# Kernel tuning notes

Hardware: AMD Instinct MI355X
Metric: run time of the kernel (lower is better)

Reference implementation:

```python
import jax, jax.numpy as jnp
import numpy as np

L, K, D, V, S, B = 2, 4, 1024, 32000, 1024, 2

# Constant neighbor influence from the 2x2 grid (success_rate==0.5 for fresh blocks)
_pos = np.array([[0, 0], [0, 1], [1, 0], [1, 1]], dtype=np.float64)
_dist = np.sqrt(((_pos[:, None, :] - _pos[None, :, :]) ** 2).sum(-1))
_infl = np.where(np.eye(K, dtype=bool), 0.0, 0.5 / (1.0 + _dist)).sum(-1)
NEIGHBOR_SIG = jnp.asarray(1.0 / (1.0 + np.exp(-_infl)), dtype=jnp.float32)  # [K]


def _ln(x, g, b, eps=1e-5):
    mu = x.mean(-1, keepdims=True)
    var = ((x - mu) ** 2).mean(-1, keepdims=True)
    return (x - mu) / jnp.sqrt(var + eps) * g + b


def setup_inputs() -> dict:
    key = jax.random.key(0)
    ks = jax.random.split(key, 10)
    def n(k, shape, s):
        return jax.random.normal(k, shape, jnp.float32) * s
    return {
        "input_ids": jax.random.randint(ks[0], (B, S), 0, V),
        "embedding": n(ks[1], (V, D), 0.02),
        "pos_enc": n(ks[2], (S, D), 0.02),
        "torsion_field": jnp.zeros((D,), jnp.float32),
        "ln1_g": jnp.ones((L, D), jnp.float32),
        "ln1_b": jnp.zeros((L, D), jnp.float32),
        "base_W": n(ks[3], (L, D, D), 0.02),
        "blk_W1": n(ks[4], (L, K, D // 2, D), 0.02),
        "blk_W2": n(ks[5], (L, K, D, D // 2), 0.02),
        "blk_gate": n(ks[6], (L, K, D), 0.01),
        "prop_W": n(ks[7], (L, K, K), 0.5),
        "prop_b": jnp.zeros((L, K), jnp.float32),
        "ln2_g": jnp.ones((L, D), jnp.float32),
        "ln2_b": jnp.zeros((L, D), jnp.float32),
        "out_ln_g": jnp.ones((D,), jnp.float32),
        "out_ln_b": jnp.zeros((D,), jnp.float32),
        "lm_head_W": n(ks[8], (V, D), 0.02),
    }


def reference(input_ids, embedding, pos_enc, torsion_field, ln1_g, ln1_b,
              base_W, blk_W1, blk_W2, blk_gate, prop_W, prop_b,
              ln2_g, ln2_b, out_ln_g, out_ln_b, lm_head_W):
    h = embedding[input_ids] + pos_enc[None]  # [B,S,D]
    s = jnp.full((K,), 0.5, h.dtype)  # fresh blocks: success_rate = 0.5
    for l in range(L):
        # excitement (detached in torch via .item())
        exc0 = jax.nn.sigmoid(prop_W[l] @ s + prop_b[l])
        exc = jax.lax.stop_gradient(0.6 * exc0 + 0.4 * NEIGHBOR_SIG)  # [K]
        hn = _ln(h, ln1_g[l], ln1_b[l])
        base = hn @ base_W[l].T  # [B,S,D]
        # all K blocks are always loaded (min_blocks == max_blocks == 4)
        t = jnp.einsum('bsd,khd->bksh', hn, blk_W1[l])
        t = jax.nn.gelu(t, approximate=False)
        t = jnp.einsum('bksh,kdh->bksd', t, blk_W2[l])
        gate = jax.nn.sigmoid(blk_gate[l] + torsion_field)  # [K,D]
        t = t * gate[None, :, None, :]
        combined = jnp.einsum('bksd,k->bsd', t, exc) / exc.sum()
        h = h + (base + combined) * 0.3
        h = _ln(h, ln2_g[l], ln2_b[l])
    h = _ln(h, out_ln_g, out_ln_b)
    return h @ lm_head_W.T  # [B,S,V]
```

## Files before the change

### kernel.cpp

```cpp
#include <hip/hip_runtime.h>
#include <math.h>

typedef unsigned short u16;
typedef short s16x8 __attribute__((ext_vector_type(8)));
typedef float f32x4 __attribute__((ext_vector_type(4)));
typedef u16 u16x4 __attribute__((ext_vector_type(4)));
typedef int i32x4 __attribute__((ext_vector_type(4)));

#define D 1024
#define MM 2048
#define HH 512
#define VV 32000

static __device__ __forceinline__ u16 f2bf(float f) {
    union { float f; unsigned int i; } c; c.f = f;
    unsigned int x = c.i;
    return (u16)((x + 0x7fffu + ((x >> 16) & 1u)) >> 16);
}
static __device__ __forceinline__ float sigm(float x) { return 1.0f / (1.0f + expf(-x)); }

static __device__ __forceinline__ void load_lds16(const u16* g, u16* l) {
    __builtin_amdgcn_global_load_lds(
        (const __attribute__((address_space(1))) unsigned int*)g,
        (__attribute__((address_space(3))) unsigned int*)l, 16, 0, 0);
}

__global__ __launch_bounds__(256) void cvt_kernel(const float* __restrict__ in,
                                                  u16* __restrict__ out, const int n4)
{
    for (int i = blockIdx.x * 256 + threadIdx.x; i < n4; i += gridDim.x * 256) {
        f32x4 v = ((const f32x4*)in)[i];
        u16x4 o;
#pragma unroll
        for (int j = 0; j < 4; j++) o[j] = f2bf(v[j]);
        ((u16x4*)out)[i] = o;
    }
}

__global__ __launch_bounds__(256) void embed_kernel(const int* __restrict__ ids,
    const float* __restrict__ emb, const float* __restrict__ pos, float* __restrict__ h)
{
    const int m = blockIdx.x;
    const int s = m & 1023;
    const long id = ids[m];
    const int d = threadIdx.x * 4;
    f32x4 ev = *(const f32x4*)&emb[id * D + d];
    f32x4 pv = *(const f32x4*)&pos[(long)s * D + d];
    f32x4 o;
#pragma unroll
    for (int i = 0; i < 4; i++) o[i] = ev[i] + pv[i];
    *(f32x4*)&h[(long)m * D + d] = o;
}

__global__ __launch_bounds__(256) void ln_bf16_kernel(const float* __restrict__ h,
    u16* __restrict__ out, const float* __restrict__ g, const float* __restrict__ b)
{
    const int row = blockIdx.x;
    const int d = threadIdx.x * 4;
    f32x4 x = *(const f32x4*)&h[(long)row * D + d];
    float s = x[0] + x[1] + x[2] + x[3];
    float ss = x[0]*x[0] + x[1]*x[1] + x[2]*x[2] + x[3]*x[3];
#pragma unroll
    for (int off = 32; off; off >>= 1) { s += __shfl_xor(s, off); ss += __shfl_xor(ss, off); }
    __shared__ float red[8];
    const int wid = threadIdx.x >> 6;
    if ((threadIdx.x & 63) == 0) { red[wid] = s; red[4 + wid] = ss; }
    __syncthreads();
    s = red[0] + red[1] + red[2] + red[3];
    ss = red[4] + red[5] + red[6] + red[7];
    const float mu = s * (1.0f / D);
    const float rstd = rsqrtf(ss * (1.0f / D) - mu * mu + 1e-5f);
    f32x4 gv = *(const f32x4*)&g[d];
    f32x4 bv = *(const f32x4*)&b[d];
    u16x4 o;
#pragma unroll
    for (int i = 0; i < 4; i++) o[i] = f2bf((x[i] - mu) * rstd * gv[i] + bv[i]);
    *(u16x4*)&out[(long)row * D + d] = o;
}

__global__ __launch_bounds__(256) void resln_kernel(float* __restrict__ h,
    const float* __restrict__ c, const float* __restrict__ g, const float* __restrict__ b)
{
    const int row = blockIdx.x;
    const int d = threadIdx.x * 4;
    f32x4 x = *(const f32x4*)&h[(long)row * D + d];
    f32x4 cv = *(const f32x4*)&c[(long)row * D + d];
#pragma unroll
    for (int i = 0; i < 4; i++) x[i] += 0.3f * cv[i];
    float s = x[0] + x[1] + x[2] + x[3];
    float ss = x[0]*x[0] + x[1]*x[1] + x[2]*x[2] + x[3]*x[3];
#pragma unroll
    for (int off = 32; off; off >>= 1) { s += __shfl_xor(s, off); ss += __shfl_xor(ss, off); }
    __shared__ float red[8];
    const int wid = threadIdx.x >> 6;
    if ((threadIdx.x & 63) == 0) { red[wid] = s; red[4 + wid] = ss; }
    __syncthreads();
    s = red[0] + red[1] + red[2] + red[3];
    ss = red[4] + red[5] + red[6] + red[7];
    const float mu = s * (1.0f / D);
    const float rstd = rsqrtf(ss * (1.0f / D) - mu * mu + 1e-5f);
    f32x4 gv = *(const f32x4*)&g[d];
    f32x4 bv = *(const f32x4*)&b[d];
    f32x4 o;
#pragma unroll
    for (int i = 0; i < 4; i++) o[i] = (x[i] - mu) * rstd * gv[i] + bv[i];
    *(f32x4*)&h[(long)row * D + d] = o;
}

__global__ void exc_kernel(const float* __restrict__ pW, const float* __restrict__ pb,
                           float* __restrict__ sc)
{
    if (threadIdx.x == 0 && blockIdx.x == 0) {
        const float NS = 1.0f / (1.0f + expf(-0.70710678118654752f));
        float e[4], sum = 0.0f;
        for (int k = 0; k < 4; k++) {
            float a = pb[k];
            for (int j = 0; j < 4; j++) a += 0.5f * pW[k * 4 + j];
            e[k] = 0.6f * sigm(a) + 0.4f * NS;
            sum += e[k];
        }
        for (int k = 0; k < 4; k++) sc[k] = e[k] / sum;
    }
}

__global__ __launch_bounds__(256) void scale_w2_kernel(
    const float* __restrict__ W2l,
    const float* __restrict__ gatel,
    const float* __restrict__ tors,
    const float* __restrict__ sc,
    u16* __restrict__ W2eff)
{
    const int n = blockIdx.x >> 1;
    const int half = blockIdx.x & 1;
    const int kh = half * 1024 + threadIdx.x * 4;
    const int k = kh >> 9;
    const int hh = kh & 511;
    const float f = sigm(gatel[k * D + n] + tors[n]) * sc[k];
    f32x4 w = *(const f32x4*)&W2l[((long)k * D + n) * HH + hh];
    u16x4 o;
#pragma unroll
    for (int i = 0; i < 4; i++) o[i] = f2bf(w[i] * f);
    *(u16x4*)&W2eff[(long)n * 2048 + kh] = o;
}

template<int EPI, int BN>
__global__ __launch_bounds__(256) void gemm_lds_kernel(
    const u16* __restrict__ A, const u16* __restrict__ W,
    float* __restrict__ Cf, u16* __restrict__ Cb,
    const int K, const long ldc, const long strideWz, const long strideCz)
{
    W += (long)blockIdx.z * strideWz;
    if (EPI == 1) Cb += (long)blockIdx.z * strideCz;
    else          Cf += (long)blockIdx.z * strideCz;

    const int gx = gridDim.x;
    const int nwg = gx * gridDim.y;
    int lin = blockIdx.y * gx + blockIdx.x;
    lin = (lin & 7) * (nwg >> 3) + (lin >> 3);
    const int bm = (lin % gx) * 128;
    const int bn = (lin / gx) * BN;

    __shared__ __align__(16) u16 As[128 * 32];
    __shared__ __align__(16) u16 Bs[BN * 32];

    const int tid = threadIdx.x;
    const int lane = tid & 63;
    const int w = tid >> 6;
    const int wm = (w >> 1) * 64;
    const int wn = (w & 1) * (BN / 2);
    const int lr = lane & 15;
    const int lkb = (lane >> 4) * 16;

    const int srow = lane >> 2;
    const int scol = (lane & 3) * 8;

    constexpr int NA = 8;
    constexpr int NB = BN / 16;
    constexpr int NIT = (NA + NB) / 4;

    f32x4 acc[4][BN / 32];
#pragma unroll
    for (int i = 0; i < 4; i++)
#pragma unroll
        for (int j = 0; j < BN / 32; j++) acc[i][j] = f32x4{0.f, 0.f, 0.f, 0.f};

    for (int k0 = 0; k0 < K; k0 += 32) {
        __syncthreads();
#pragma unroll
        for (int it = 0; it < NIT; ++it) {
            const int c = w + it * 4;
            if (c < NA) {
                load_lds16(&A[(long)(bm + c * 16 + srow) * K + k0 + scol], &As[c * 512]);
            } else {
                const int c2 = c - NA;
                load_lds16(&W[(long)(bn + c2 * 16 + srow) * K + k0 + scol], &Bs[c2 * 512]);
            }
        }
        __syncthreads();
        s16x8 a[4], b[BN / 32];
#pragma unroll
        for (int i = 0; i < 4; i++)
            a[i] = *(const s16x8*)((const char*)As + (wm + i * 16 + lr) * 64 + lkb);
#pragma unroll
        for (int j = 0; j < BN / 32; j++)
            b[j] = *(const s16x8*)((const char*)Bs + (wn + j * 16 + lr) * 64 + lkb);
#pragma unroll
        for (int i = 0; i < 4; i++)
#pragma unroll
            for (int j = 0; j < BN / 32; j++)
                acc[i][j] = __builtin_amdgcn_mfma_f32_16x16x32_bf16(a[i], b[j], acc[i][j], 0, 0, 0);
    }

    const int r0 = (lane >> 4) * 4;
#pragma unroll
    for (int i = 0; i < 4; i++) {
#pragma unroll
        for (int j = 0; j < BN / 32; j++) {
            const int n = bn + wn + j * 16 + lr;
#pragma unroll
            for (int r = 0; r < 4; r++) {
                const int m = bm + wm + i * 16 + r0 + r;
                const float v = acc[i][j][r];
                if (EPI == 0) {
                    Cf[(long)m * ldc + n] = v;
                } else if (EPI == 1) {
                    const float gel = 0.5f * v * (1.0f + erff(v * 0.70710678118654752f));
                    Cb[(long)m * ldc + n] = f2bf(gel);
                } else {
                    Cf[(long)m * ldc + n] += v;
                }
            }
        }
    }
}

extern "C" void kernel_launch(void* const* d_in, const int* in_sizes, int n_in,
                              void* d_out, int out_size, void* d_ws, size_t ws_size,
                              hipStream_t stream)
{
    (void)in_sizes; (void)n_in; (void)out_size; (void)ws_size;
    const int*   ids   = (const int*)d_in[0];
    const float* emb   = (const float*)d_in[1];
    const float* pos   = (const float*)d_in[2];
    const float* tors  = (const float*)d_in[3];
    const float* ln1g  = (const float*)d_in[4];
    const float* ln1b  = (const float*)d_in[5];
    const float* baseW = (const float*)d_in[6];
    const float* W1    = (const float*)d_in[7];
    const float* W2    = (const float*)d_in[8];
    const float* gate  = (const float*)d_in[9];
    const float* propW = (const float*)d_in[10];
    const float* propb = (const float*)d_in[11];
    const float* ln2g  = (const float*)d_in[12];
    const float* ln2b  = (const float*)d_in[13];
    const float* outg  = (const float*)d_in[14];
    const float* outb  = (const float*)d_in[15];
    const float* lmW   = (const float*)d_in[16];

    char* ws = (char*)d_ws;
    float* h     = (float*)(ws);
    u16*   hn    = (u16*)  (ws + (8l  << 20));
    u16*   bWbf  = (u16*)  (ws + (12l << 20));
    u16*   W1bf  = (u16*)  (ws + (14l << 20));
    float* C     = (float*)(ws + (18l << 20));
    u16*   t     = (u16*)  (ws + (26l << 20));
    u16*   W2eff = (u16*)  (ws + (34l << 20));
    float* sc    = (float*)(ws + (38l << 20));
    u16*   lmWbf = (u16*)  (ws + (12l << 20));

    embed_kernel<<<MM, 256, 0, stream>>>(ids, emb, pos, h);

    for (int l = 0; l < 2; l++) {
        exc_kernel<<<1, 64, 0, stream>>>(propW + l * 16, propb + l * 4, sc);
        ln_bf16_kernel<<<MM, 256, 0, stream>>>(h, hn, ln1g + (long)l * D, ln1b + (long)l * D);
        cvt_kernel<<<1024, 256, 0, stream>>>(baseW + (long)l * D * D, bWbf, D * D / 4);
        cvt_kernel<<<2048, 256, 0, stream>>>(W1 + (long)l * 4 * HH * D, W1bf, 4 * HH * D / 4);
        gemm_lds_kernel<0, 64><<<dim3(16, 16, 1), 256, 0, stream>>>(
            hn, bWbf, C, nullptr, D, D, 0, 0);
        gemm_lds_kernel<1, 64><<<dim3(16, 8, 4), 256, 0, stream>>>(
            hn, W1bf, nullptr, t, D, 2048, (long)HH * D, 512);
        scale_w2_kernel<<<2048, 256, 0, stream>>>(
            W2 + (long)l * 4 * D * HH, gate + (long)l * 4 * D, tors, sc, W2eff);
        gemm_lds_kernel<2, 64><<<dim3(16, 16, 1), 256, 0, stream>>>(
            t, W2eff, C, nullptr, 2048, D, 0, 0);
        resln_kernel<<<MM, 256, 0, stream>>>(h, C, ln2g + (long)l * D, ln2b + (long)l * D);
    }

    ln_bf16_kernel<<<MM, 256, 0, stream>>>(h, hn, outg, outb);
    cvt_kernel<<<2048, 256, 0, stream>>>(lmW, lmWbf, VV * D / 4);
    gemm_lds_kernel<0, 128><<<dim3(16, 250, 1), 256, 0, stream>>>(
        hn, lmWbf, (float*)d_out, nullptr, D, VV, 0, 0);
}
```

Before: 438.7 us.

## Add 256x256 pipelined LDS GEMM with XCD-aware tiling for LM head

Replaces the generic LM-head GEMM with a dedicated 512-thread kernel that computes 256x256 output tiles. It uses eight XOR-swizzled LDS slots with a ping-pong schedule that interleaves global-to-LDS loads with MFMA phases, plus s_setprio and explicit vmcnt waits. The block index is remapped so neighbouring tiles land on the same XCD, improving L2 reuse. The goal is higher MFMA utilisation and fewer stalls on the dominant 2048x32000x1024 GEMM, at the cost of hard-coded shapes and a large register footprint.

```diff
diff --git a/kernel.cpp b/kernel.cpp
--- a/kernel.cpp
+++ b/kernel.cpp
@@ -124,10 +124,8 @@
 }
 
 __global__ __launch_bounds__(256) void scale_w2_kernel(
-    const float* __restrict__ W2l,
-    const float* __restrict__ gatel,
-    const float* __restrict__ tors,
-    const float* __restrict__ sc,
+    const float* __restrict__ W2l, const float* __restrict__ gatel,
+    const float* __restrict__ tors, const float* __restrict__ sc,
     u16* __restrict__ W2eff)
 {
     const int n = blockIdx.x >> 1;
@@ -232,6 +230,111 @@
             }
         }
     }
+}
+
+
+static __device__ __forceinline__ void stageHalf(u16* slot, const u16* g, int wid, int lane) {
+    const int r = wid * 16 + (lane >> 2);
+    const int c16 = (lane & 3) ^ ((lane >> 2) & 3);
+    load_lds16(g + (long)r * 1024 + c16 * 8, slot + wid * 512);
+}
+static __device__ __forceinline__ s16x8 ldsFrag(const u16* slot, int fr, int lane) {
+    const int row = fr + (lane & 15);
+    const int c16 = (lane >> 4) ^ (row & 3);
+    return *(const s16x8*)(slot + row * 32 + c16 * 8);
+}
+
+#define SLOT(ab, buf, half) (lds[((ab) << 2) | ((buf) << 1) | (half)])
+#define VMCNT2() asm volatile("s_waitcnt vmcnt(2)" ::: "memory")
+#define SBAR()   do { __builtin_amdgcn_s_barrier(); __builtin_amdgcn_sched_barrier(0); } while (0)
+
+#define PHASE(qm, qn, rb, STAGE_STMT, DO_VM)                                        \
+    do {                                                                            \
+        s16x8 af[2], bf[4];                                                         \
+        _Pragma("unroll") for (int ii = 0; ii < 2; ++ii)                            \
+            af[ii] = ldsFrag(SLOT(0, rb, qm), fmBase + ii * 16, lane);              \
+        _Pragma("unroll") for (int jj = 0; jj < 4; ++jj)                            \
+            bf[jj] = ldsFrag(SLOT(1, rb, qn), fnBase + jj * 16, lane);              \
+        STAGE_STMT;                                                                 \
+        SBAR();                                                                     \
+        __builtin_amdgcn_s_setprio(1);                                              \
+        _Pragma("unroll") for (int ii = 0; ii < 2; ++ii)                            \
+            _Pragma("unroll") for (int jj = 0; jj < 4; ++jj)                        \
+                acc[qm][qn][ii][jj] = __builtin_amdgcn_mfma_f32_16x16x32_bf16(      \
+                    af[ii], bf[jj], acc[qm][qn][ii][jj], 0, 0, 0);                  \
+        __builtin_amdgcn_s_setprio(0);                                              \
+        if (DO_VM) VMCNT2();                                                        \
+        SBAR();                                                                     \
+    } while (0)
+
+__global__ __launch_bounds__(512, 2) void gemm256_kernel(
+    const u16* __restrict__ Ag, const u16* __restrict__ Wg, float* __restrict__ C)
+{
+    const int nwg = gridDim.x * gridDim.y;
+    int lin = blockIdx.y * gridDim.x + blockIdx.x;
+    lin = (lin & 7) * (nwg >> 3) + (lin >> 3);
+    const int bm = (lin & 7) * 256;
+    const int bn = (lin >> 3) * 256;
+
+    __shared__ __align__(16) u16 lds[8][128 * 32];
+
+    const int tid = threadIdx.x;
+    const int lane = tid & 63;
+    const int w = tid >> 6;
+    const int fmBase = (w & 3) * 32;
+    const int fnBase = (w >> 2) * 64;
+
+    f32x4 acc[2][2][2][4];
+#pragma unroll
+    for (int a0 = 0; a0 < 2; ++a0)
+#pragma unroll
+        for (int a1 = 0; a1 < 2; ++a1)
+#pragma unroll
+            for (int a2 = 0; a2 < 2; ++a2)
+#pragma unroll
+                for (int a3 = 0; a3 < 4; ++a3) acc[a0][a1][a2][a3] = f32x4{0.f, 0.f, 0.f, 0.f};
+
+    stageHalf(SLOT(0, 0, 0), Ag + (long)(bm      ) * 1024,      w, lane);
+    stageHalf(SLOT(1, 0, 0), Wg + (long)(bn      ) * 1024,      w, lane);
+    stageHalf(SLOT(0, 0, 1), Ag + (long)(bm + 128) * 1024,      w, lane);
+    stageHalf(SLOT(1, 0, 1), Wg + (long)(bn + 128) * 1024,      w, lane);
+    stageHalf(SLOT(1, 1, 0), Wg + (long)(bn      ) * 1024 + 32, w, lane);
+    stageHalf(SLOT(0, 1, 0), Ag + (long)(bm      ) * 1024 + 32, w, lane);
+    VMCNT2();
+    SBAR();
+
+    for (int i = 0; i < 16; ++i) {
+        const int t = 2 * i;
+        const long k1 = (long)(t + 1) * 32;
+        const long k2 = (long)((t + 2) & 31) * 32;
+        const long k3 = (long)((t + 3) & 31) * 32;
+
+        PHASE(0, 0, 0, stageHalf(SLOT(0, 1, 1), Ag + (long)(bm + 128) * 1024 + k1, w, lane), 0);
+        PHASE(1, 0, 0, stageHalf(SLOT(1, 1, 1), Wg + (long)(bn + 128) * 1024 + k1, w, lane), 0);
+        PHASE(0, 1, 0, stageHalf(SLOT(1, 0, 0), Wg + (long)(bn      ) * 1024 + k2, w, lane), 0);
+        PHASE(1, 1, 0, stageHalf(SLOT(0, 0, 0), Ag + (long)(bm      ) * 1024 + k2, w, lane), 1);
+        PHASE(0, 0, 1, stageHalf(SLOT(0, 0, 1), Ag + (long)(bm + 128) * 1024 + k2, w, lane), 0);
+        PHASE(1, 0, 1, stageHalf(SLOT(1, 0, 1), Wg + (long)(bn + 128) * 1024 + k2, w, lane), 0);
+        PHASE(0, 1, 1, stageHalf(SLOT(1, 1, 0), Wg + (long)(bn      ) * 1024 + k3, w, lane), 0);
+        PHASE(1, 1, 1, stageHalf(SLOT(0, 1, 0), Ag + (long)(bm      ) * 1024 + k3, w, lane), 1);
+    }
+
+    const int r0 = (lane >> 4) * 4;
+    const int cl = lane & 15;
+#pragma unroll
+    for (int qm = 0; qm < 2; ++qm)
+#pragma unroll
+        for (int qn = 0; qn < 2; ++qn)
+#pragma unroll
+            for (int ii = 0; ii < 2; ++ii)
+#pragma unroll
+                for (int jj = 0; jj < 4; ++jj) {
+                    const int m = bm + qm * 128 + fmBase + ii * 16 + r0;
+                    const int n = bn + qn * 128 + fnBase + jj * 16 + cl;
+#pragma unroll
+                    for (int rr = 0; rr < 4; ++rr)
+                        C[(long)(m + rr) * VV + n] = acc[qm][qn][ii][jj][rr];
+                }
 }
 
 extern "C" void kernel_launch(void* const* d_in, const int* in_sizes, int n_in,
@@ -288,6 +391,5 @@
 
     ln_bf16_kernel<<<MM, 256, 0, stream>>>(h, hn, outg, outb);
     cvt_kernel<<<2048, 256, 0, stream>>>(lmW, lmWbf, VV * D / 4);
-    gemm_lds_kernel<0, 128><<<dim3(16, 250, 1), 256, 0, stream>>>(
-        hn, lmWbf, (float*)d_out, nullptr, D, VV, 0, 0);
-}
+    gemm256_kernel<<<dim3(8, 125), 512, 0, stream>>>(hn, lmWbf, (float*)d_out);
+}
```

Result: slower. 451.7 us (+3.0%).

## Add 256x256-tile pipelined MFMA GEMM for the LM head projection

Applied to the files above, without the earlier changes.

Replaces the generic 128-wide LDS GEMM used for the final vocab projection with a dedicated 512-thread kernel. Each workgroup computes a 256x256 output tile using double-buffered global-to-LDS loads interleaved with MFMA phases. It also adds priority raising around the MFMA phases and a swizzled workgroup order for L2 reuse. The larger tiles cut global re-reads of the 2048x1024 activations and 32000x1024 weights, in exchange for a 128 KB LDS footprint, higher register pressure and many barriers per k-tile. The new kernel is hardcoded to M=2048, K=1024 and N=32000.

```diff
diff --git a/kernel.cpp b/kernel.cpp
--- a/kernel.cpp
+++ b/kernel.cpp
@@ -124,10 +124,8 @@
 }
 
 __global__ __launch_bounds__(256) void scale_w2_kernel(
-    const float* __restrict__ W2l,
-    const float* __restrict__ gatel,
-    const float* __restrict__ tors,
-    const float* __restrict__ sc,
+    const float* __restrict__ W2l, const float* __restrict__ gatel,
+    const float* __restrict__ tors, const float* __restrict__ sc,
     u16* __restrict__ W2eff)
 {
     const int n = blockIdx.x >> 1;
@@ -232,6 +230,139 @@
             }
         }
     }
+}
+
+
+#define AU16  16384
+#define HALFU 8192
+#define BB0   32768
+
+#define BAR() do { __builtin_amdgcn_s_barrier(); __builtin_amdgcn_sched_barrier(0); } while (0)
+
+__global__ __launch_bounds__(512, 2) void gemm256_kernel(
+    const u16* __restrict__ Ag, const u16* __restrict__ Wg, float* __restrict__ C)
+{
+    __shared__ __align__(16) u16 lds[65536];
+
+    const int nwg = gridDim.x * gridDim.y;
+    int lin = blockIdx.y * gridDim.x + blockIdx.x;
+    lin = (lin & 7) * (nwg >> 3) + (lin >> 3);
+    const int bm = (lin & 7) * 256;
+    const int bn = (lin >> 3) * 256;
+
+    const int tid = threadIdx.x;
+    const int lane = tid & 63;
+    const int w = tid >> 6;
+    const int wm = w >> 2;
+    const int wn = w & 3;
+
+    const u16* aSrc = Ag + (long)(bm + w * 16 + (lane & 15)) * 1024 + ((lane >> 4) * 8);
+    const u16* bSrc = Wg + (long)(bn + w * 16 + (lane & 15)) * 1024 + ((lane >> 4) * 8);
+    u16* aDst = lds + w * 1024;
+    u16* bDst = lds + BB0 + w * 1024;
+
+    auto stageA = [&](int kt, int b, int kk) {
+        const long co = (long)kt * 64 + kk * 32;
+        load_lds16(aSrc + co,               aDst + b * AU16 + kk * 512);
+        load_lds16(aSrc + co + 128 * 1024L, aDst + b * AU16 + HALFU + kk * 512);
+    };
+    auto stageB = [&](int kt, int b, int kk) {
+        const long co = (long)kt * 64 + kk * 32;
+        load_lds16(bSrc + co,               bDst + b * AU16 + kk * 512);
+        load_lds16(bSrc + co + 128 * 1024L, bDst + b * AU16 + HALFU + kk * 512);
+    };
+
+    const u16* aRd = lds + wm * HALFU + lane * 8;
+    const u16* bRd = lds + BB0 + (wn >> 1) * HALFU + (wn & 1) * 4096 + lane * 8;
+
+    f32x4 acc[8][4];
+#pragma unroll
+    for (int i = 0; i < 8; ++i)
+#pragma unroll
+        for (int j = 0; j < 4; ++j) acc[i][j] = f32x4{0.f, 0.f, 0.f, 0.f};
+
+    stageA(0, 0, 0); stageB(0, 0, 0); stageA(0, 0, 1); stageB(0, 0, 1);
+    stageA(1, 1, 0); stageB(1, 1, 0); stageA(1, 1, 1);
+    asm volatile("s_waitcnt vmcnt(6)" ::: "memory");
+    BAR();
+
+    auto ktile = [&](int t, int b) {
+        const int t1 = (t + 1) & 15, t2 = (t + 2) & 15;
+        s16x8 af[8], bf[2];
+#pragma unroll
+        for (int i = 0; i < 8; ++i) af[i] = *(const s16x8*)(aRd + b * AU16 + i * 1024);
+#pragma unroll
+        for (int j = 0; j < 2; ++j) bf[j] = *(const s16x8*)(bRd + b * AU16 + j * 1024);
+        stageB(t1, b ^ 1, 1);
+        BAR();
+        __builtin_amdgcn_s_setprio(1);
+#pragma unroll
+        for (int i = 0; i < 8; ++i) {
+            acc[i][0] = __builtin_amdgcn_mfma_f32_16x16x32_bf16(af[i], bf[0], acc[i][0], 0, 0, 0);
+            acc[i][1] = __builtin_amdgcn_mfma_f32_16x16x32_bf16(af[i], bf[1], acc[i][1], 0, 0, 0);
+        }
+        __builtin_amdgcn_s_setprio(0);
+        BAR();
+#pragma unroll
+        for (int j = 0; j < 2; ++j) bf[j] = *(const s16x8*)(bRd + b * AU16 + 2048 + j * 1024);
+        stageA(t2, b, 0);
+        BAR();
+        __builtin_amdgcn_s_setprio(1);
+#pragma unroll
+        for (int i = 0; i < 8; ++i) {
+            acc[i][2] = __builtin_amdgcn_mfma_f32_16x16x32_bf16(af[i], bf[0], acc[i][2], 0, 0, 0);
+            acc[i][3] = __builtin_amdgcn_mfma_f32_16x16x32_bf16(af[i], bf[1], acc[i][3], 0, 0, 0);
+        }
+        __builtin_amdgcn_s_setprio(0);
+        BAR();
+#pragma unroll
+        for (int i = 0; i < 8; ++i) af[i] = *(const s16x8*)(aRd + b * AU16 + i * 1024 + 512);
+#pragma unroll
+        for (int j = 0; j < 2; ++j) bf[j] = *(const s16x8*)(bRd + b * AU16 + j * 1024 + 512);
+        stageB(t2, b, 0);
+        BAR();
+        __builtin_amdgcn_s_setprio(1);
+#pragma unroll
+        for (int i = 0; i < 8; ++i) {
+            acc[i][0] = __builtin_amdgcn_mfma_f32_16x16x32_bf16(af[i], bf[0], acc[i][0], 0, 0, 0);
+            acc[i][1] = __builtin_amdgcn_mfma_f32_16x16x32_bf16(af[i], bf[1], acc[i][1], 0, 0, 0);
+        }
+        __builtin_amdgcn_s_setprio(0);
+        BAR();
+#pragma unroll
+        for (int j = 0; j < 2; ++j) bf[j] = *(const s16x8*)(bRd + b * AU16 + 2048 + j * 1024 + 512);
+        stageA(t2, b, 1);
+        BAR();
+        __builtin_amdgcn_s_setprio(1);
+#pragma unroll
+        for (int i = 0; i < 8; ++i) {
+            acc[i][2] = __builtin_amdgcn_mfma_f32_16x16x32_bf16(af[i], bf[0], acc[i][2], 0, 0, 0);
+            acc[i][3] = __builtin_amdgcn_mfma_f32_16x16x32_bf16(af[i], bf[1], acc[i][3], 0, 0, 0);
+        }
+        __builtin_amdgcn_s_setprio(0);
+        asm volatile("s_waitcnt vmcnt(6)" ::: "memory");
+        BAR();
+    };
+
+    for (int tt = 0; tt < 8; ++tt) {
+        ktile(2 * tt,     0);
+        ktile(2 * tt + 1, 1);
+    }
+
+    asm volatile("s_waitcnt vmcnt(0)" ::: "memory");
+
+    const int r0 = (lane >> 4) * 4;
+    const int cl = lane & 15;
+#pragma unroll
+    for (int i = 0; i < 8; ++i)
+#pragma unroll
+        for (int j = 0; j < 4; ++j) {
+            const long m = bm + wm * 128 + i * 16 + r0;
+            const int n = bn + wn * 64 + j * 16 + cl;
+#pragma unroll
+            for (int rr = 0; rr < 4; ++rr)
+                C[(m + rr) * (long)VV + n] = acc[i][j][rr];
+        }
 }
 
 extern "C" void kernel_launch(void* const* d_in, const int* in_sizes, int n_in,
@@ -288,6 +419,5 @@
 
     ln_bf16_kernel<<<MM, 256, 0, stream>>>(h, hn, outg, outb);
     cvt_kernel<<<2048, 256, 0, stream>>>(lmW, lmWbf, VV * D / 4);
-    gemm_lds_kernel<0, 128><<<dim3(16, 250, 1), 256, 0, stream>>>(
-        hn, lmWbf, (float*)d_out, nullptr, D, VV, 0, 0);
-}
+    gemm256_kernel<<<dim3(8, 125), 512, 0, stream>>>(hn, lmWbf, (float*)d_out);
+}
```

Result: no change. 442.8 us (+0.9%).

## Fuse base and W1 GEMMs, split-K W2 GEMM with atomics, stage LM-head stores

Applied to the files above, without the earlier changes.

Base_W and W1 are concatenated into one bf16 weight, converted in a single kernel, and multiplied in one 128x128-tile GEMM whose epilogue writes fp32 base output or GELU'd bf16 activations depending on the column. The W2 GEMM is split along K into 4 z-slices that accumulate into C with atomicAdd, which raises parallelism. The LM-head GEMM now uses 128-wide N tiles everywhere and stages output through LDS so it can issue vectorized float4 stores. The LDS load layout also changes so each lane loads a contiguous 16-byte chunk. Together these cut launches and improve tile efficiency, at the cost of atomic contention and nondeterministic summation order.

```diff
diff --git a/kernel.cpp b/kernel.cpp
--- a/kernel.cpp
+++ b/kernel.cpp
@@ -5,7 +5,6 @@
 typedef short s16x8 __attribute__((ext_vector_type(8)));
 typedef float f32x4 __attribute__((ext_vector_type(4)));
 typedef u16 u16x4 __attribute__((ext_vector_type(4)));
-typedef int i32x4 __attribute__((ext_vector_type(4)));
 
 #define D 1024
 #define MM 2048
@@ -30,6 +29,19 @@
 {
     for (int i = blockIdx.x * 256 + threadIdx.x; i < n4; i += gridDim.x * 256) {
         f32x4 v = ((const f32x4*)in)[i];
+        u16x4 o;
+#pragma unroll
+        for (int j = 0; j < 4; j++) o[j] = f2bf(v[j]);
+        ((u16x4*)out)[i] = o;
+    }
+}
+
+__global__ __launch_bounds__(256) void cvtcat_kernel(const float* __restrict__ baseW,
+    const float* __restrict__ W1, u16* __restrict__ out)
+{
+    const int N4 = 3072 * 1024 / 4, B4 = 1024 * 1024 / 4;
+    for (int i = blockIdx.x * 256 + threadIdx.x; i < N4; i += gridDim.x * 256) {
+        f32x4 v = (i < B4) ? ((const f32x4*)baseW)[i] : ((const f32x4*)W1)[i - B4];
         u16x4 o;
 #pragma unroll
         for (int j = 0; j < 4; j++) o[j] = f2bf(v[j]);
@@ -124,10 +136,8 @@
 }
 
 __global__ __launch_bounds__(256) void scale_w2_kernel(
-    const float* __restrict__ W2l,
-    const float* __restrict__ gatel,
-    const float* __restrict__ tors,
-    const float* __restrict__ sc,
+    const float* __restrict__ W2l, const float* __restrict__ gatel,
+    const float* __restrict__ tors, const float* __restrict__ sc,
     u16* __restrict__ W2eff)
 {
     const int n = blockIdx.x >> 1;
@@ -143,91 +153,97 @@
     *(u16x4*)&W2eff[(long)n * 2048 + kh] = o;
 }
 
-template<int EPI, int BN>
-__global__ __launch_bounds__(256) void gemm_lds_kernel(
+template<int EPI>
+__global__ __launch_bounds__(256) void gemm_t(
     const u16* __restrict__ A, const u16* __restrict__ W,
     float* __restrict__ Cf, u16* __restrict__ Cb,
-    const int K, const long ldc, const long strideWz, const long strideCz)
-{
-    W += (long)blockIdx.z * strideWz;
-    if (EPI == 1) Cb += (long)blockIdx.z * strideCz;
-    else          Cf += (long)blockIdx.z * strideCz;
+    const int Kloop, const int ldk, const long ldc)
+{
+    if (EPI == 4) { A += blockIdx.z * 512; W += blockIdx.z * 512; }
 
     const int gx = gridDim.x;
     const int nwg = gx * gridDim.y;
     int lin = blockIdx.y * gx + blockIdx.x;
     lin = (lin & 7) * (nwg >> 3) + (lin >> 3);
     const int bm = (lin % gx) * 128;
-    const int bn = (lin / gx) * BN;
-
-    __shared__ __align__(16) u16 As[128 * 32];
-    __shared__ __align__(16) u16 Bs[BN * 32];
-
-    const int tid = threadIdx.x;
-    const int lane = tid & 63;
-    const int w = tid >> 6;
-    const int wm = (w >> 1) * 64;
-    const int wn = (w & 1) * (BN / 2);
-    const int lr = lane & 15;
-    const int lkb = (lane >> 4) * 16;
-
-    const int srow = lane >> 2;
-    const int scol = (lane & 3) * 8;
-
-    constexpr int NA = 8;
-    constexpr int NB = BN / 16;
-    constexpr int NIT = (NA + NB) / 4;
-
-    f32x4 acc[4][BN / 32];
-#pragma unroll
-    for (int i = 0; i < 4; i++)
-#pragma unroll
-        for (int j = 0; j < BN / 32; j++) acc[i][j] = f32x4{0.f, 0.f, 0.f, 0.f};
-
-    for (int k0 = 0; k0 < K; k0 += 32) {
+    const int bn = (lin / gx) * 128;
+
+    __shared__ __align__(16) u16 AB[8192];
+    __shared__ float epi[(EPI == 0 ? 4 : 1)][16][72];
+
+    const int tid = threadIdx.x, lane = tid & 63, w = tid >> 6;
+    const int wm = w >> 1, wn = w & 1;
+    const int l15 = lane & 15, lk8 = (lane >> 4) * 8;
+
+    const u16* src[4];
+    u16* dst[4];
+#pragma unroll
+    for (int ci = 0; ci < 4; ++ci) {
+        const int c = w + ci * 4;
+        src[ci] = (c < 8 ? A + (long)(bm + c * 16 + l15) * ldk
+                         : W + (long)(bn + (c - 8) * 16 + l15) * ldk) + lk8;
+        dst[ci] = AB + c * 512;
+    }
+
+    f32x4 acc[4][4];
+#pragma unroll
+    for (int i = 0; i < 4; ++i)
+#pragma unroll
+        for (int j = 0; j < 4; ++j) acc[i][j] = f32x4{0.f, 0.f, 0.f, 0.f};
+
+    for (int k0 = 0; k0 < Kloop; k0 += 32) {
         __syncthreads();
 #pragma unroll
-        for (int it = 0; it < NIT; ++it) {
-            const int c = w + it * 4;
-            if (c < NA) {
-                load_lds16(&A[(long)(bm + c * 16 + srow) * K + k0 + scol], &As[c * 512]);
-            } else {
-                const int c2 = c - NA;
-                load_lds16(&W[(long)(bn + c2 * 16 + srow) * K + k0 + scol], &Bs[c2 * 512]);
+        for (int ci = 0; ci < 4; ++ci) load_lds16(src[ci] + k0, dst[ci]);
+        __syncthreads();
+        s16x8 a[4], b[4];
+#pragma unroll
+        for (int i = 0; i < 4; ++i) a[i] = *(const s16x8*)(AB + (wm * 4 + i) * 512 + lane * 8);
+#pragma unroll
+        for (int j = 0; j < 4; ++j) b[j] = *(const s16x8*)(AB + (8 + wn * 4 + j) * 512 + lane * 8);
+#pragma unroll
+        for (int i = 0; i < 4; ++i)
+#pragma unroll
+            for (int j = 0; j < 4; ++j)
+                acc[i][j] = __builtin_amdgcn_mfma_f32_16x16x32_bf16(a[i], b[j], acc[i][j], 0, 0, 0);
+    }
+
+    const int r0 = (lane >> 4) * 4;
+    if (EPI == 0) {
+#pragma unroll
+        for (int i = 0; i < 4; ++i) {
+#pragma unroll
+            for (int j = 0; j < 4; ++j)
+#pragma unroll
+                for (int rr = 0; rr < 4; ++rr)
+                    epi[w][r0 + rr][j * 16 + l15] = acc[i][j][rr];
+#pragma unroll
+            for (int p = 0; p < 4; ++p) {
+                const int r16 = p * 4 + (lane >> 4);
+                f32x4 v = *(const f32x4*)&epi[w][r16][l15 * 4];
+                *(f32x4*)&Cf[(long)(bm + wm * 64 + i * 16 + r16) * ldc + bn + wn * 64 + l15 * 4] = v;
             }
         }
-        __syncthreads();
-        s16x8 a[4], b[BN / 32];
-#pragma unroll
-        for (int i = 0; i < 4; i++)
-            a[i] = *(const s16x8*)((const char*)As + (wm + i * 16 + lr) * 64 + lkb);
-#pragma unroll
-        for (int j = 0; j < BN / 32; j++)
-            b[j] = *(const s16x8*)((const char*)Bs + (wn + j * 16 + lr) * 64 + lkb);
-#pragma unroll
-        for (int i = 0; i < 4; i++)
-#pragma unroll
-            for (int j = 0; j < BN / 32; j++)
-                acc[i][j] = __builtin_amdgcn_mfma_f32_16x16x32_bf16(a[i], b[j], acc[i][j], 0, 0, 0);
-    }
-
-    const int r0 = (lane >> 4) * 4;
-#pragma unroll
-    for (int i = 0; i < 4; i++) {
-#pragma unroll
-        for (int j = 0; j < BN / 32; j++) {
-            const int n = bn + wn + j * 16 + lr;
-#pragma unroll
-            for (int r = 0; r < 4; r++) {
-                const int m = bm + wm + i * 16 + r0 + r;
-                const float v = acc[i][j][r];
-                if (EPI == 0) {
-                    Cf[(long)m * ldc + n] = v;
-                } else if (EPI == 1) {
-                    const float gel = 0.5f * v * (1.0f + erff(v * 0.70710678118654752f));
-                    Cb[(long)m * ldc + n] = f2bf(gel);
-                } else {
-                    Cf[(long)m * ldc + n] += v;
+    } else {
+#pragma unroll
+        for (int i = 0; i < 4; ++i) {
+#pragma unroll
+            for (int j = 0; j < 4; ++j) {
+                const int n = bn + wn * 64 + j * 16 + l15;
+#pragma unroll
+                for (int rr = 0; rr < 4; ++rr) {
+                    const int m = bm + wm * 64 + i * 16 + r0 + rr;
+                    const float v = acc[i][j][rr];
+                    if (EPI == 3) {
+                        if (n < 1024) {
+                            Cf[(long)m * 1024 + n] = v;
+                        } else {
+                            const float gel = 0.5f * v * (1.0f + erff(v * 0.70710678118654752f));
+                            Cb[(long)m * 2048 + (n - 1024)] = f2bf(gel);
+                        }
+                    } else {
+                        atomicAdd(&Cf[(long)m * ldc + n], v);
+                    }
                 }
             }
         }
@@ -260,8 +276,7 @@
     char* ws = (char*)d_ws;
     float* h     = (float*)(ws);
     u16*   hn    = (u16*)  (ws + (8l  << 20));
-    u16*   bWbf  = (u16*)  (ws + (12l << 20));
-    u16*   W1bf  = (u16*)  (ws + (14l << 20));
+    u16*   Wcat  = (u16*)  (ws + (12l << 20));
     float* C     = (float*)(ws + (18l << 20));
     u16*   t     = (u16*)  (ws + (26l << 20));
     u16*   W2eff = (u16*)  (ws + (34l << 20));
@@ -273,21 +288,19 @@
     for (int l = 0; l < 2; l++) {
         exc_kernel<<<1, 64, 0, stream>>>(propW + l * 16, propb + l * 4, sc);
         ln_bf16_kernel<<<MM, 256, 0, stream>>>(h, hn, ln1g + (long)l * D, ln1b + (long)l * D);
-        cvt_kernel<<<1024, 256, 0, stream>>>(baseW + (long)l * D * D, bWbf, D * D / 4);
-        cvt_kernel<<<2048, 256, 0, stream>>>(W1 + (long)l * 4 * HH * D, W1bf, 4 * HH * D / 4);
-        gemm_lds_kernel<0, 64><<<dim3(16, 16, 1), 256, 0, stream>>>(
-            hn, bWbf, C, nullptr, D, D, 0, 0);
-        gemm_lds_kernel<1, 64><<<dim3(16, 8, 4), 256, 0, stream>>>(
-            hn, W1bf, nullptr, t, D, 2048, (long)HH * D, 512);
+        cvtcat_kernel<<<1024, 256, 0, stream>>>(
+            baseW + (long)l * D * D, W1 + (long)l * 4 * HH * D, Wcat);
         scale_w2_kernel<<<2048, 256, 0, stream>>>(
             W2 + (long)l * 4 * D * HH, gate + (long)l * 4 * D, tors, sc, W2eff);
-        gemm_lds_kernel<2, 64><<<dim3(16, 16, 1), 256, 0, stream>>>(
-            t, W2eff, C, nullptr, 2048, D, 0, 0);
+        gemm_t<3><<<dim3(16, 24), 256, 0, stream>>>(
+            hn, Wcat, C, t, 1024, 1024, 0);
+        gemm_t<4><<<dim3(16, 8, 4), 256, 0, stream>>>(
+            t, W2eff, C, nullptr, 512, 2048, 1024);
         resln_kernel<<<MM, 256, 0, stream>>>(h, C, ln2g + (long)l * D, ln2b + (long)l * D);
     }
 
     ln_bf16_kernel<<<MM, 256, 0, stream>>>(h, hn, outg, outb);
     cvt_kernel<<<2048, 256, 0, stream>>>(lmW, lmWbf, VV * D / 4);
-    gemm_lds_kernel<0, 128><<<dim3(16, 250, 1), 256, 0, stream>>>(
-        hn, lmWbf, (float*)d_out, nullptr, D, VV, 0, 0);
-}
+    gemm_t<0><<<dim3(16, 250), 256, 0, stream>>>(
+        hn, lmWbf, (float*)d_out, nullptr, 1024, 1024, VV);
+}
```

Result: slower. 525.7 us (+19.8%).
